# Optimization experiments

Hardware: AMD Instinct MI355X
Metric: run time of the kernel (lower is better)

The kernel has to match this reference:

```python
import jax, jax.numpy as jnp
import numpy as np

H = 16  # num_heads

def setup_inputs() -> dict:
    key = jax.random.key(0)
    ks = jax.random.split(key, 6)
    B, N, D = 2, 2048, 1024
    s = 0.02
    return {
        "x": jax.random.normal(ks[0], (B, N, D), jnp.float32),
        "attn_bias": jax.random.normal(ks[1], (B, N), jnp.float32),
        "w_qkv": jax.random.normal(ks[2], (D, 3 * D), jnp.float32) * s,
        "b_qkv": jnp.zeros((3 * D,), jnp.float32),
        "w_proj": jax.random.normal(ks[3], (D, D), jnp.float32) * s,
        "b_proj": jnp.zeros((D,), jnp.float32),
    }

def reference(x, attn_bias, w_qkv, b_qkv, w_proj, b_proj):
    B, N, D = x.shape
    hd = D // H
    qkv = x @ w_qkv + b_qkv                       # (B,N,3D)
    qkv = qkv.reshape(B, N, 3, H, hd)
    q, k, v = qkv[:, :, 0], qkv[:, :, 1], qkv[:, :, 2]  # (B,N,H,hd)
    scores = jnp.einsum("bqhd,bkhd->bhqk", q, k) / np.sqrt(hd).astype(x.dtype)
    scores = scores + attn_bias[:, None, None, :]  # key-wise bias (B,1,1,N)
    w = jax.nn.softmax(scores, axis=-1)
    out = jnp.einsum("bhqk,bkhd->bqhd", w, v).reshape(B, N, D)
    return out @ w_proj + b_proj
```

## Files before the change

### kernel.cpp

```cpp
#include <hip/hip_runtime.h>
#include <stdint.h>

typedef __attribute__((ext_vector_type(8))) short bf16x8;
typedef __attribute__((ext_vector_type(4))) short s16x4;
typedef __attribute__((ext_vector_type(4))) float f32x4;
typedef __attribute__((ext_vector_type(4))) unsigned int u32x4;

#define DEV __device__ __forceinline__

DEV unsigned short f2bf(float f) {
    unsigned u = __builtin_bit_cast(unsigned, f);
    u += 0x7FFFu + ((u >> 16) & 1u);
    return (unsigned short)(u >> 16);
}

DEV void gload_lds16(const void* g, void* l) {
    __builtin_amdgcn_global_load_lds(
        (const __attribute__((address_space(1))) unsigned int*)g,
        (__attribute__((address_space(3))) unsigned int*)l,
        16, 0, 0);
}

__global__ __launch_bounds__(256) void cvt_f32_bf16(
    const float* __restrict__ in, unsigned short* __restrict__ out, int n4) {
    int i = blockIdx.x * blockDim.x + threadIdx.x;
    if (i >= n4) return;
    const float4 v = reinterpret_cast<const float4*>(in)[i];
    s16x4 o;
    o.x = (short)f2bf(v.x); o.y = (short)f2bf(v.y);
    o.z = (short)f2bf(v.z); o.w = (short)f2bf(v.w);
    reinterpret_cast<s16x4*>(out)[i] = o;
}

__global__ __launch_bounds__(256) void transpose_w(
    const float* __restrict__ w, unsigned short* __restrict__ wt, int K, int N) {
    __shared__ unsigned short tile[64][72];
    const int k0 = blockIdx.y * 64, n0 = blockIdx.x * 64;
    const int t = threadIdx.x;
    #pragma unroll
    for (int i = 0; i < 4; ++i) {
        const int e = t + i * 256;
        const int r = e >> 4, c4 = e & 15;
        const float4 v = *reinterpret_cast<const float4*>(w + (size_t)(k0 + r) * N + n0 + c4 * 4);
        s16x4 o;
        o.x = (short)f2bf(v.x); o.y = (short)f2bf(v.y);
        o.z = (short)f2bf(v.z); o.w = (short)f2bf(v.w);
        *(s16x4*)&tile[r][c4 * 4] = o;
    }
    __syncthreads();
    #pragma unroll
    for (int i = 0; i < 4; ++i) {
        const int e = t + i * 256;
        const int rn = e >> 4, c4 = e & 15;
        s16x4 o;
        o.x = (short)tile[c4 * 4 + 0][rn];
        o.y = (short)tile[c4 * 4 + 1][rn];
        o.z = (short)tile[c4 * 4 + 2][rn];
        o.w = (short)tile[c4 * 4 + 3][rn];
        *(s16x4*)(wt + (size_t)(n0 + rn) * K + k0 + c4 * 4) = o;
    }
}

__global__ __launch_bounds__(512, 2)
void gemm256_qkv(const unsigned short* __restrict__ A,
                 const unsigned short* __restrict__ BT,
                 const float* __restrict__ bias,
                 unsigned short* __restrict__ q_out,
                 unsigned short* __restrict__ k_out,
                 unsigned short* __restrict__ v_out)
{
    constexpr int K = 1024;
    constexpr int NT = 16;
    __shared__ unsigned short lds[2][2][2][2][128][32];

    const int t = threadIdx.x;
    const int wave = t >> 6, lane = t & 63;
    const int l15 = lane & 15, l4 = lane >> 4;
    const int wr = wave >> 2, wc = wave & 3;

    const int lin = blockIdx.x;
    const int logical = (lin & 7) * 24 + (lin >> 3);
    const int bx = logical % 12, by = logical / 12;
    const int tile_m = by * 256, tile_n = bx * 256;

    const int st_row = t >> 2;
    const int st_col = ((t & 3) ^ ((t >> 3) & 3)) * 8;
    const int cswz   = (l4 ^ ((l15 >> 1) & 3)) * 8;

    f32x4 acc[8][4] = {};
    bf16x8 ra[4], rb[4];

    #define STAGE(buf, ab, half, kk, k0)                                           \
        gload_lds16(((ab) ? BT : A) +                                              \
                        (size_t)(((ab) ? tile_n : tile_m) + (half) * 128 + st_row) * K \
                        + (k0) + (kk) * 32 + st_col,                               \
                    &lds[buf][ab][half][kk][0][0] + wave * 512)
    #define READ_A(buf, kk, mq)                                                    \
        _Pragma("unroll") for (int i = 0; i < 4; ++i)                              \
            ra[i] = *(const bf16x8*)&lds[buf][0][wr][kk][((mq) * 4 + i) * 16 + l15][cswz];
    #define READ_B(buf, kk)                                                        \
        _Pragma("unroll") for (int n = 0; n < 4; ++n)                              \
            rb[n] = *(const bf16x8*)&lds[buf][1][wc >> 1][kk][(wc & 1) * 64 + n * 16 + l15][cswz];
    #define MFMA16(mq)                                                             \
        __builtin_amdgcn_s_setprio(1);                                             \
        _Pragma("unroll") for (int i = 0; i < 4; ++i)                              \
            _Pragma("unroll") for (int n = 0; n < 4; ++n)                          \
                acc[(mq) * 4 + i][n] = __builtin_amdgcn_mfma_f32_16x16x32_bf16(    \
                    ra[i], rb[n], acc[(mq) * 4 + i][n], 0, 0, 0);                  \
        __builtin_amdgcn_s_setprio(0);
    #define BAR()   __builtin_amdgcn_s_barrier()
    #define LGKM0() do { asm volatile("s_waitcnt lgkmcnt(0)" ::: "memory");        \
                         __builtin_amdgcn_sched_barrier(0); } while (0)

    STAGE(0, 1, 0, 0, 0);  STAGE(0, 1, 1, 0, 0);
    STAGE(0, 0, 0, 0, 0);  STAGE(0, 0, 1, 0, 0);
    STAGE(0, 1, 0, 1, 0);  STAGE(0, 1, 1, 1, 0);
    STAGE(0, 0, 0, 1, 0);  STAGE(0, 0, 1, 1, 0);
    STAGE(1, 1, 0, 0, 64); STAGE(1, 1, 1, 0, 64);
    STAGE(1, 0, 0, 0, 64); STAGE(1, 0, 1, 0, 64);
    STAGE(1, 1, 0, 1, 64); STAGE(1, 1, 1, 1, 64);
    asm volatile("s_waitcnt vmcnt(6)" ::: "memory");
    BAR();

    for (int kt = 0; kt < NT; ++kt) {
        const int buf = kt & 1;
        const int k0 = kt * 64;
        const bool s1 = (kt + 1 < NT);
        const bool s234 = (kt + 2 < NT);

        READ_A(buf, 0, 0); READ_B(buf, 0);
        if (s1) { STAGE(buf ^ 1, 0, 0, 1, k0 + 64); STAGE(buf ^ 1, 0, 1, 1, k0 + 64); }
        BAR(); LGKM0();
        MFMA16(0);
        BAR();

        READ_A(buf, 0, 1);
        if (s234) { STAGE(buf, 1, 0, 0, k0 + 128); STAGE(buf, 1, 1, 0, k0 + 128); }
        BAR(); LGKM0();
        MFMA16(1);
        BAR();

        READ_A(buf, 1, 0); READ_B(buf, 1);
        if (s234) { STAGE(buf, 0, 0, 0, k0 + 128); STAGE(buf, 0, 1, 0, k0 + 128); }
        BAR(); LGKM0();
        MFMA16(0);
        BAR();

        READ_A(buf, 1, 1);
        if (s234) { STAGE(buf, 1, 0, 1, k0 + 128); STAGE(buf, 1, 1, 1, k0 + 128); }
        BAR(); LGKM0();
        MFMA16(1);
        if (kt < NT - 2)       asm volatile("s_waitcnt vmcnt(6)" ::: "memory");
        else if (kt == NT - 2) asm volatile("s_waitcnt vmcnt(0)" ::: "memory");
        if (kt < NT - 1) BAR();
    }
    #undef STAGE
    #undef READ_A
    #undef READ_B
    #undef MFMA16
    #undef BAR
    #undef LGKM0

    float bcol[4];
    #pragma unroll
    for (int n = 0; n < 4; ++n) bcol[n] = bias[tile_n + wc * 64 + n * 16 + l15];

    #pragma unroll
    for (int m = 0; m < 8; ++m)
        #pragma unroll
        for (int n = 0; n < 4; ++n) {
            const int col = tile_n + wc * 64 + n * 16 + l15;
            const int which = col >> 10;
            const int hh = (col >> 6) & 15;
            const int d = col & 63;
            const int row0 = tile_m + wr * 128 + m * 16 + l4 * 4;
            const int bb = row0 >> 11, nn = row0 & 2047;
            if (which == 2) {
                const int nl = nn & 63;
                const int np = (nl & 32) | ((nl & 12) << 1) | ((nl & 16) >> 2) | (nl & 3);
                const size_t dstV = ((size_t)((bb * 16 + hh) * 64 + d)) * 2048 + (nn & ~63) + np;
                s16x4 pk;
                #pragma unroll
                for (int r = 0; r < 4; ++r) pk[r] = (short)f2bf(acc[m][n][r] + bcol[n]);
                *(s16x4*)&v_out[dstV] = pk;
            } else {
                #pragma unroll
                for (int r = 0; r < 4; ++r) {
                    const float v = acc[m][n][r] + bcol[n];
                    const size_t dst = ((size_t)((bb * 16 + hh) * 2048 + nn + r)) * 64 + d;
                    if (which == 0) q_out[dst] = f2bf(v * 0.125f);
                    else            k_out[dst] = f2bf(v);
                }
            }
        }
}

__global__ __launch_bounds__(256)
void gemm_bf16_f32out(const unsigned short* __restrict__ A,
                      const unsigned short* __restrict__ BT,
                      const float* __restrict__ bias,
                      float* __restrict__ f_out,
                      int M, int N, int K)
{
    __shared__ unsigned short Abuf[128 * 64];
    __shared__ unsigned short Bbuf[128 * 64];

    const int t = threadIdx.x;
    const int wave = t >> 6, lane = t & 63;
    const int l15 = lane & 15, l4 = lane >> 4;
    const int wr = wave >> 1, wc = wave & 1;
    const int tile_m = blockIdx.y * 128, tile_n = blockIdx.x * 128;

    const int srow = wave * 32 + (lane >> 3);
    const int scol = (lane & 7) * 8;

    f32x4 acc[4][4] = {};

    const int nk = K >> 6;
    for (int kt = 0; kt < nk; ++kt) {
        const int k0 = kt << 6;
        __syncthreads();
        #pragma unroll
        for (int c = 0; c < 4; ++c) {
            const unsigned short* sa = A + (size_t)(tile_m + srow + c * 8) * K + k0 + scol;
            gload_lds16(sa, &Abuf[(wave * 32 + c * 8) * 64]);
            const unsigned short* sb = BT + (size_t)(tile_n + srow + c * 8) * K + k0 + scol;
            gload_lds16(sb, &Bbuf[(wave * 32 + c * 8) * 64]);
        }
        asm volatile("s_waitcnt vmcnt(0)" ::: "memory");
        __syncthreads();

        bf16x8 ra[4][2], rb[4][2];
        #pragma unroll
        for (int m = 0; m < 4; ++m)
            #pragma unroll
            for (int ks = 0; ks < 2; ++ks)
                ra[m][ks] = *(const bf16x8*)&Abuf[(wr * 64 + m * 16 + l15) * 64 + ks * 32 + l4 * 8];
        #pragma unroll
        for (int n = 0; n < 4; ++n)
            #pragma unroll
            for (int ks = 0; ks < 2; ++ks)
                rb[n][ks] = *(const bf16x8*)&Bbuf[(wc * 64 + n * 16 + l15) * 64 + ks * 32 + l4 * 8];

        #pragma unroll
        for (int m = 0; m < 4; ++m)
            #pragma unroll
            for (int n = 0; n < 4; ++n) {
                acc[m][n] = __builtin_amdgcn_mfma_f32_16x16x32_bf16(ra[m][0], rb[n][0], acc[m][n], 0, 0, 0);
                acc[m][n] = __builtin_amdgcn_mfma_f32_16x16x32_bf16(ra[m][1], rb[n][1], acc[m][n], 0, 0, 0);
            }
    }

    float bcol[4];
    #pragma unroll
    for (int n = 0; n < 4; ++n) bcol[n] = bias[tile_n + wc * 64 + n * 16 + l15];

    #pragma unroll
    for (int m = 0; m < 4; ++m)
        #pragma unroll
        for (int n = 0; n < 4; ++n) {
            const int col = tile_n + wc * 64 + n * 16 + l15;
            #pragma unroll
            for (int r = 0; r < 4; ++r) {
                const int row = tile_m + wr * 64 + m * 16 + l4 * 4 + r;
                f_out[(size_t)row * N + col] = acc[m][n][r] + bcol[n];
            }
        }
}

__global__ __launch_bounds__(1024, 8)
void attn_kernel(const unsigned short* __restrict__ Qb,
                 const unsigned short* __restrict__ Kb,
                 const unsigned short* __restrict__ Vt,
                 const float* __restrict__ bias,
                 unsigned short* __restrict__ Ob)
{
    __shared__ __align__(16) unsigned char pool[73728];
    unsigned short (*Kf)[4096] = (unsigned short (*)[4096])(pool);
    unsigned short (*Vf)[4096] = (unsigned short (*)[4096])(pool + 32768);
    float* blds = (float*)(pool + 65536);
    float (*Oscr)[16][64] = (float (*)[16][64])(pool);
    float (*Lscr)[8][16]  = (float (*)[8][16])(pool + 32768);

    const unsigned di = blockIdx.x;
    const unsigned logical = (di & 7) * 64 + (di >> 3);
    const int qt = logical & 15;
    const int h  = (logical >> 4) & 15;
    const int b  = logical >> 8;

    const int t = threadIdx.x;
    const int wave = t >> 6, lane = t & 63;
    const int l15 = lane & 15, l4 = lane >> 4;
    const int wq = wave >> 1, wk = wave & 1;
    const int kb0 = wk * 32;
    const int xsw = (l15 & 7) << 3;

    const size_t head = ((size_t)(b * 16 + h)) * 2048 * 64;
    const unsigned short* Qh = Qb + head;
    const unsigned short* Kh = Kb + head;

    const int w8 = wave & 7;
    const int srow8 = w8 * 8 + (lane >> 3);
    const int scol8 = 8 * ((lane & 7) ^ (lane >> 3));
    const unsigned short* Src = (wave < 8)
        ? Kh + (size_t)srow8 * 64 + scol8
        : Vt + ((size_t)((b * 16 + h) * 64) + srow8) * 2048 + scol8;
    const int sstep = (wave < 8) ? 64 * 64 : 64;
    unsigned short* lbase = (wave < 8) ? &Kf[0][w8 * 512] : &Vf[0][w8 * 512];

    for (int i = t; i < 2048; i += 1024) blds[i] = bias[b * 2048 + i] - 5.5451774f;

    const int qbase = qt * 128 + wq * 16;
    bf16x8 qf[2];
    #pragma unroll
    for (int ks = 0; ks < 2; ++ks)
        qf[ks] = *(const bf16x8*)(Qh + (size_t)(qbase + l15) * 64 + ks * 32 + l4 * 8);

    float lsum = 0.f;
    f32x4 oacc[4] = {};

    gload_lds16(Src, lbase);
    gload_lds16(Src + sstep, lbase + 4096);
    __syncthreads();

    for (int kt = 0; kt < 32; ++kt) {
        const int key0 = kt * 64;
        const int pb = kt & 3;

        if (kt < 30)
            gload_lds16(Src + (size_t)(kt + 2) * sstep, lbase + ((kt + 2) & 3) * 4096);

        if (kt < 30)       asm volatile("s_waitcnt vmcnt(2)" ::: "memory");
        else if (kt == 30) asm volatile("s_waitcnt vmcnt(1)" ::: "memory");
        else               asm volatile("s_waitcnt vmcnt(0)" ::: "memory");
        __builtin_amdgcn_s_barrier();
        __builtin_amdgcn_sched_barrier(0);

        const unsigned short* Kp = Kf[pb];
        const unsigned short* Vp = Vf[pb];

        bf16x8 kfr[2][2];
        #pragma unroll
        for (int f = 0; f < 2; ++f)
            #pragma unroll
            for (int ks = 0; ks < 2; ++ks)
                kfr[f][ks] = *(const bf16x8*)&Kp[(kb0 + f * 16 + l15) * 64 + ((ks * 32 + l4 * 8) ^ xsw)];

        f32x4 bk[2];
        #pragma unroll
        for (int f = 0; f < 2; ++f)
            bk[f] = *(const f32x4*)&blds[key0 + kb0 + f * 16 + l4 * 4];

        f32x4 s[2];
        __builtin_amdgcn_s_setprio(1);
        #pragma unroll
        for (int f = 0; f < 2; ++f) {
            f32x4 z = bk[f];
            z = __builtin_amdgcn_mfma_f32_16x16x32_bf16(kfr[f][0], qf[0], z, 0, 0, 0);
            z = __builtin_amdgcn_mfma_f32_16x16x32_bf16(kfr[f][1], qf[1], z, 0, 0, 0);
            s[f] = z;
        }
        __builtin_amdgcn_s_setprio(0);

        float ps = 0.f;
        u32x4 w;
        #pragma unroll
        for (int f = 0; f < 2; ++f) {
            const float p0 = __expf(s[f][0]);
            const float p1 = __expf(s[f][1]);
            const float p2 = __expf(s[f][2]);
            const float p3 = __expf(s[f][3]);
            ps += (p0 + p1) + (p2 + p3);
            unsigned w0, w1;
            asm("v_cvt_pk_bf16_f32 %0, %1, %2" : "=v"(w0) : "v"(p0), "v"(p1));
            asm("v_cvt_pk_bf16_f32 %0, %1, %2" : "=v"(w1) : "v"(p2), "v"(p3));
            w[f * 2] = w0; w[f * 2 + 1] = w1;
        }
        lsum += ps;
        const bf16x8 pa = __builtin_bit_cast(bf16x8, w);

        __builtin_amdgcn_s_setprio(1);
        #pragma unroll
        for (int df = 0; df < 4; ++df) {
            bf16x8 vf = *(const bf16x8*)&Vp[(df * 16 + l15) * 64 + ((kb0 + l4 * 8) ^ xsw)];
            oacc[df] = __builtin_amdgcn_mfma_f32_16x16x32_bf16(pa, vf, oacc[df], 0, 0, 0);
        }
        __builtin_amdgcn_s_setprio(0);
    }

    lsum += __shfl_xor(lsum, 16, 64);
    lsum += __shfl_xor(lsum, 32, 64);

    __syncthreads();
    if (lane < 16) Lscr[wk][wq][lane] = lsum;
    if (wk == 1) {
        #pragma unroll
        for (int df = 0; df < 4; ++df)
            #pragma unroll
            for (int r = 0; r < 4; ++r)
                Oscr[wq][l4 * 4 + r][df * 16 + l15] = oacc[df][r];
    }
    __syncthreads();
    if (wk == 0) {
        float inv[4];
        #pragma unroll
        for (int r = 0; r < 4; ++r) {
            const int ql = l4 * 4 + r;
            inv[r] = 1.0f / (Lscr[0][wq][ql] + Lscr[1][wq][ql]);
        }
        #pragma unroll
        for (int r = 0; r < 4; ++r) {
            const int ql = l4 * 4 + r;
            const int q = qbase + ql;
            #pragma unroll
            for (int df = 0; df < 4; ++df) {
                const int d = df * 16 + l15;
                const float v = oacc[df][r] + Oscr[wq][ql][d];
                Ob[((size_t)(b * 2048 + q)) * 1024 + h * 64 + d] = f2bf(v * inv[r]);
            }
        }
    }
}

extern "C" void kernel_launch(void* const* d_in, const int* in_sizes, int n_in,
                              void* d_out, int out_size, void* d_ws, size_t ws_size,
                              hipStream_t stream) {
    const float* x      = (const float*)d_in[0];
    const float* abias  = (const float*)d_in[1];
    const float* w_qkv  = (const float*)d_in[2];
    const float* b_qkv  = (const float*)d_in[3];
    const float* w_proj = (const float*)d_in[4];
    const float* b_proj = (const float*)d_in[5];
    float* out = (float*)d_out;

    unsigned short* ws = (unsigned short*)d_ws;
    unsigned short* xb  = ws;
    unsigned short* wqT = xb  + (size_t)4096 * 1024;
    unsigned short* wpT = wqT + (size_t)3072 * 1024;
    unsigned short* qb  = wpT + (size_t)1024 * 1024;
    unsigned short* kb  = qb  + (size_t)2 * 16 * 2048 * 64;
    unsigned short* vt  = kb  + (size_t)2 * 16 * 2048 * 64;
    unsigned short* ao  = vt  + (size_t)2 * 16 * 2048 * 64;

    cvt_f32_bf16<<<4096, 256, 0, stream>>>(x, xb, 1048576);
    transpose_w<<<dim3(48, 16), 256, 0, stream>>>(w_qkv, wqT, 1024, 3072);
    transpose_w<<<dim3(16, 16), 256, 0, stream>>>(w_proj, wpT, 1024, 1024);
    gemm256_qkv<<<192, 512, 0, stream>>>(xb, wqT, b_qkv, qb, kb, vt);
    attn_kernel<<<512, 1024, 0, stream>>>(qb, kb, vt, abias, ao);
    gemm_bf16_f32out<<<dim3(8, 32), 256, 0, stream>>>(ao, wpT, b_proj, out, 4096, 1024, 1024);
}
```

Baseline: 125.0 us.

## Process two key tiles per barrier in attention and shrink proj GEMM tiles

```diff
diff --git a/kernel.cpp b/kernel.cpp
--- a/kernel.cpp
+++ b/kernel.cpp
@@ -196,54 +196,54 @@
 }
 
 __global__ __launch_bounds__(256)
-void gemm_bf16_f32out(const unsigned short* __restrict__ A,
-                      const unsigned short* __restrict__ BT,
-                      const float* __restrict__ bias,
-                      float* __restrict__ f_out,
-                      int M, int N, int K)
+void gemm_proj(const unsigned short* __restrict__ A,
+               const unsigned short* __restrict__ BT,
+               const float* __restrict__ bias,
+               float* __restrict__ f_out)
 {
+    constexpr int K = 1024, N = 1024;
     __shared__ unsigned short Abuf[128 * 64];
-    __shared__ unsigned short Bbuf[128 * 64];
+    __shared__ unsigned short Bbuf[64 * 64];
 
     const int t = threadIdx.x;
     const int wave = t >> 6, lane = t & 63;
     const int l15 = lane & 15, l4 = lane >> 4;
-    const int wr = wave >> 1, wc = wave & 1;
-    const int tile_m = blockIdx.y * 128, tile_n = blockIdx.x * 128;
+    const int tile_n = blockIdx.x * 64, tile_m = blockIdx.y * 128;
 
     const int srow = wave * 32 + (lane >> 3);
+    const int brow = t >> 3;
     const int scol = (lane & 7) * 8;
 
-    f32x4 acc[4][4] = {};
-
-    const int nk = K >> 6;
-    for (int kt = 0; kt < nk; ++kt) {
+    f32x4 acc[2][4] = {};
+
+    for (int kt = 0; kt < 16; ++kt) {
         const int k0 = kt << 6;
         __syncthreads();
         #pragma unroll
-        for (int c = 0; c < 4; ++c) {
-            const unsigned short* sa = A + (size_t)(tile_m + srow + c * 8) * K + k0 + scol;
-            gload_lds16(sa, &Abuf[(wave * 32 + c * 8) * 64]);
-            const unsigned short* sb = BT + (size_t)(tile_n + srow + c * 8) * K + k0 + scol;
-            gload_lds16(sb, &Bbuf[(wave * 32 + c * 8) * 64]);
-        }
+        for (int c = 0; c < 4; ++c)
+            gload_lds16(A + (size_t)(tile_m + srow + c * 8) * K + k0 + scol,
+                        &Abuf[(wave * 32 + c * 8) * 64]);
+        #pragma unroll
+        for (int c = 0; c < 2; ++c)
+            gload_lds16(BT + (size_t)(tile_n + brow + c * 32) * K + k0 + scol,
+                        &Bbuf[(c * 32 + wave * 8) * 64]);
         asm volatile("s_waitcnt vmcnt(0)" ::: "memory");
         __syncthreads();
 
-        bf16x8 ra[4][2], rb[4][2];
-        #pragma unroll
-        for (int m = 0; m < 4; ++m)
+        bf16x8 ra[2][2], rb[4][2];
+        #pragma unroll
+        for (int m = 0; m < 2; ++m)
             #pragma unroll
             for (int ks = 0; ks < 2; ++ks)
-                ra[m][ks] = *(const bf16x8*)&Abuf[(wr * 64 + m * 16 + l15) * 64 + ks * 32 + l4 * 8];
+                ra[m][ks] = *(const bf16x8*)&Abuf[(wave * 32 + m * 16 + l15) * 64 + ks * 32 + l4 * 8];
         #pragma unroll
         for (int n = 0; n < 4; ++n)
             #pragma unroll
             for (int ks = 0; ks < 2; ++ks)
-                rb[n][ks] = *(const bf16x8*)&Bbuf[(wc * 64 + n * 16 + l15) * 64 + ks * 32 + l4 * 8];
-
-        #pragma unroll
-        for (int m = 0; m < 4; ++m)
+                rb[n][ks] = *(const bf16x8*)&Bbuf[(n * 16 + l15) * 64 + ks * 32 + l4 * 8];
+
+        #pragma unroll
+        for (int m = 0; m < 2; ++m)
             #pragma unroll
             for (int n = 0; n < 4; ++n) {
                 acc[m][n] = __builtin_amdgcn_mfma_f32_16x16x32_bf16(ra[m][0], rb[n][0], acc[m][n], 0, 0, 0);
@@ -253,16 +253,16 @@
 
     float bcol[4];
     #pragma unroll
-    for (int n = 0; n < 4; ++n) bcol[n] = bias[tile_n + wc * 64 + n * 16 + l15];
-
-    #pragma unroll
-    for (int m = 0; m < 4; ++m)
+    for (int n = 0; n < 4; ++n) bcol[n] = bias[tile_n + n * 16 + l15];
+
+    #pragma unroll
+    for (int m = 0; m < 2; ++m)
         #pragma unroll
         for (int n = 0; n < 4; ++n) {
-            const int col = tile_n + wc * 64 + n * 16 + l15;
+            const int col = tile_n + n * 16 + l15;
             #pragma unroll
             for (int r = 0; r < 4; ++r) {
-                const int row = tile_m + wr * 64 + m * 16 + l4 * 4 + r;
+                const int row = tile_m + wave * 32 + m * 16 + l4 * 4 + r;
                 f_out[(size_t)row * N + col] = acc[m][n][r] + bcol[n];
             }
         }
@@ -323,69 +323,67 @@
     gload_lds16(Src + sstep, lbase + 4096);
     __syncthreads();
 
-    for (int kt = 0; kt < 32; ++kt) {
-        const int key0 = kt * 64;
-        const int pb = kt & 3;
-
-        if (kt < 30)
-            gload_lds16(Src + (size_t)(kt + 2) * sstep, lbase + ((kt + 2) & 3) * 4096);
-
-        if (kt < 30)       asm volatile("s_waitcnt vmcnt(2)" ::: "memory");
-        else if (kt == 30) asm volatile("s_waitcnt vmcnt(1)" ::: "memory");
-        else               asm volatile("s_waitcnt vmcnt(0)" ::: "memory");
+    for (int kt = 0; kt < 32; kt += 2) {
+        asm volatile("s_waitcnt vmcnt(0)" ::: "memory");
         __builtin_amdgcn_s_barrier();
         __builtin_amdgcn_sched_barrier(0);
 
-        const unsigned short* Kp = Kf[pb];
-        const unsigned short* Vp = Vf[pb];
-
-        bf16x8 kfr[2][2];
-        #pragma unroll
-        for (int f = 0; f < 2; ++f)
-            #pragma unroll
-            for (int ks = 0; ks < 2; ++ks)
-                kfr[f][ks] = *(const bf16x8*)&Kp[(kb0 + f * 16 + l15) * 64 + ((ks * 32 + l4 * 8) ^ xsw)];
-
-        f32x4 bk[2];
-        #pragma unroll
-        for (int f = 0; f < 2; ++f)
-            bk[f] = *(const f32x4*)&blds[key0 + kb0 + f * 16 + l4 * 4];
-
-        f32x4 s[2];
-        __builtin_amdgcn_s_setprio(1);
-        #pragma unroll
-        for (int f = 0; f < 2; ++f) {
-            f32x4 z = bk[f];
-            z = __builtin_amdgcn_mfma_f32_16x16x32_bf16(kfr[f][0], qf[0], z, 0, 0, 0);
-            z = __builtin_amdgcn_mfma_f32_16x16x32_bf16(kfr[f][1], qf[1], z, 0, 0, 0);
-            s[f] = z;
-        }
-        __builtin_amdgcn_s_setprio(0);
-
-        float ps = 0.f;
-        u32x4 w;
-        #pragma unroll
-        for (int f = 0; f < 2; ++f) {
-            const float p0 = __expf(s[f][0]);
-            const float p1 = __expf(s[f][1]);
-            const float p2 = __expf(s[f][2]);
-            const float p3 = __expf(s[f][3]);
-            ps += (p0 + p1) + (p2 + p3);
-            unsigned w0, w1;
-            asm("v_cvt_pk_bf16_f32 %0, %1, %2" : "=v"(w0) : "v"(p0), "v"(p1));
-            asm("v_cvt_pk_bf16_f32 %0, %1, %2" : "=v"(w1) : "v"(p2), "v"(p3));
-            w[f * 2] = w0; w[f * 2 + 1] = w1;
-        }
-        lsum += ps;
-        const bf16x8 pa = __builtin_bit_cast(bf16x8, w);
-
-        __builtin_amdgcn_s_setprio(1);
-        #pragma unroll
-        for (int df = 0; df < 4; ++df) {
-            bf16x8 vf = *(const bf16x8*)&Vp[(df * 16 + l15) * 64 + ((kb0 + l4 * 8) ^ xsw)];
-            oacc[df] = __builtin_amdgcn_mfma_f32_16x16x32_bf16(pa, vf, oacc[df], 0, 0, 0);
-        }
-        __builtin_amdgcn_s_setprio(0);
+        if (kt < 30) {
+            gload_lds16(Src + (size_t)(kt + 2) * sstep, lbase + ((kt + 2) & 3) * 4096);
+            gload_lds16(Src + (size_t)(kt + 3) * sstep, lbase + ((kt + 3) & 3) * 4096);
+        }
+
+        #pragma unroll
+        for (int u = 0; u < 2; ++u) {
+            const int tb = (kt + u) & 3;
+            const int key0 = (kt + u) * 64;
+            const unsigned short* Kp = Kf[tb];
+            const unsigned short* Vp = Vf[tb];
+
+            bf16x8 kfr[2][2];
+            #pragma unroll
+            for (int f = 0; f < 2; ++f)
+                #pragma unroll
+                for (int ks = 0; ks < 2; ++ks)
+                    kfr[f][ks] = *(const bf16x8*)&Kp[(kb0 + f * 16 + l15) * 64 + ((ks * 32 + l4 * 8) ^ xsw)];
+
+            f32x4 bk[2];
+            #pragma unroll
+            for (int f = 0; f < 2; ++f)
+                bk[f] = *(const f32x4*)&blds[key0 + kb0 + f * 16 + l4 * 4];
+
+            f32x4 s[2];
+            #pragma unroll
+            for (int f = 0; f < 2; ++f) {
+                f32x4 z = bk[f];
+                z = __builtin_amdgcn_mfma_f32_16x16x32_bf16(kfr[f][0], qf[0], z, 0, 0, 0);
+                z = __builtin_amdgcn_mfma_f32_16x16x32_bf16(kfr[f][1], qf[1], z, 0, 0, 0);
+                s[f] = z;
+            }
+
+            float ps = 0.f;
+            u32x4 w;
+            #pragma unroll
+            for (int f = 0; f < 2; ++f) {
+                const float p0 = __expf(s[f][0]);
+                const float p1 = __expf(s[f][1]);
+                const float p2 = __expf(s[f][2]);
+                const float p3 = __expf(s[f][3]);
+                ps += (p0 + p1) + (p2 + p3);
+                unsigned w0, w1;
+                asm("v_cvt_pk_bf16_f32 %0, %1, %2" : "=v"(w0) : "v"(p0), "v"(p1));
+                asm("v_cvt_pk_bf16_f32 %0, %1, %2" : "=v"(w1) : "v"(p2), "v"(p3));
+                w[f * 2] = w0; w[f * 2 + 1] = w1;
+            }
+            lsum += ps;
+            const bf16x8 pa = __builtin_bit_cast(bf16x8, w);
+
+            #pragma unroll
+            for (int df = 0; df < 4; ++df) {
+                bf16x8 vf = *(const bf16x8*)&Vp[(df * 16 + l15) * 64 + ((kb0 + l4 * 8) ^ xsw)];
+                oacc[df] = __builtin_amdgcn_mfma_f32_16x16x32_bf16(pa, vf, oacc[df], 0, 0, 0);
+            }
+        }
     }
 
     lsum += __shfl_xor(lsum, 16, 64);
@@ -447,5 +445,5 @@
     transpose_w<<<dim3(16, 16), 256, 0, stream>>>(w_proj, wpT, 1024, 1024);
     gemm256_qkv<<<192, 512, 0, stream>>>(xb, wqT, b_qkv, qb, kb, vt);
     attn_kernel<<<512, 1024, 0, stream>>>(qb, kb, vt, abias, ao);
-    gemm_bf16_f32out<<<dim3(8, 32), 256, 0, stream>>>(ao, wpT, b_proj, out, 4096, 1024, 1024);
-}
+    gemm_proj<<<dim3(16, 32), 256, 0, stream>>>(ao, wpT, b_proj, out);
+}
```

Result: no change. 125.3 us (+0.2%).
